# Kernel tuning notes

Measured on AMD Instinct MI355X. Metric: run time of the kernel, lower is better.

Reference implementation:

```python
import jax, jax.numpy as jnp
import numpy as np

B, T, N, NIN = 2, 10, 128, 6
K, H = 4, 128          # edge_types, n_hid
E = N * (N - 1)        # fully-connected, no self-loops


def _linear_init(key, out_f, in_f, bias=True):
    k1, k2 = jax.random.split(key)
    bound = 1.0 / np.sqrt(in_f)
    W = jax.random.uniform(k1, (out_f, in_f), jnp.float32, -bound, bound)
    if bias:
        b = jax.random.uniform(k2, (out_f,), jnp.float32, -bound, bound)
        return W, b
    return W


def setup_inputs() -> dict:
    key = jax.random.key(0)
    ks = jax.random.split(key, 20)
    # graph structure: one-hot receiver/sender matrices (NRI style)
    off_diag = np.ones((N, N), dtype=np.float32) - np.eye(N, dtype=np.float32)
    send_idx, recv_idx = np.where(off_diag)
    eye = np.eye(N, dtype=np.float32)
    rel_rec = jnp.asarray(eye[recv_idx])   # [E, N]
    rel_send = jnp.asarray(eye[send_idx])  # [E, N]

    data = jax.random.normal(ks[0], (B, T, N, NIN), jnp.float32)
    rel_type = jax.nn.softmax(jax.random.normal(ks[1], (B, E, K), jnp.float32), axis=-1)

    # per-edge-type message MLPs, stacked over edge type
    m1 = [_linear_init(ks[2 + i], H, 2 * H) for i in range(K)]
    m2 = [_linear_init(ks[6 + i], H, H) for i in range(K)]
    W_msg1 = jnp.stack([w for w, _ in m1]); b_msg1 = jnp.stack([b for _, b in m1])
    W_msg2 = jnp.stack([w for w, _ in m2]); b_msg2 = jnp.stack([b for _, b in m2])

    W_hr = _linear_init(ks[10], H, H, bias=False)
    W_hi = _linear_init(ks[11], H, H, bias=False)
    W_hh = _linear_init(ks[12], H, H, bias=False)
    W_ir, b_ir = _linear_init(ks[13], H, NIN)
    W_ii, b_ii = _linear_init(ks[14], H, NIN)
    W_in, b_in = _linear_init(ks[15], H, NIN)
    W_o1, b_o1 = _linear_init(ks[16], H, H)
    W_o2, b_o2 = _linear_init(ks[17], H, H)
    W_o3, b_o3 = _linear_init(ks[18], NIN, H)

    return dict(data=data, rel_type=rel_type, rel_rec=rel_rec, rel_send=rel_send,
                W_msg1=W_msg1, b_msg1=b_msg1, W_msg2=W_msg2, b_msg2=b_msg2,
                W_hr=W_hr, W_hi=W_hi, W_hh=W_hh,
                W_ir=W_ir, b_ir=b_ir, W_ii=W_ii, b_ii=b_ii, W_in=W_in, b_in=b_in,
                W_o1=W_o1, b_o1=b_o1, W_o2=W_o2, b_o2=b_o2, W_o3=W_o3, b_o3=b_o3)


def reference(data, rel_type, rel_rec, rel_send,
              W_msg1, b_msg1, W_msg2, b_msg2,
              W_hr, W_hi, W_hh,
              W_ir, b_ir, W_ii, b_ii, W_in, b_in,
              W_o1, b_o1, W_o2, b_o2, W_o3, b_o3):
    norm = float(K)  # skip_first=False -> all edge types, norm = edge_types
    rel_type_k = jnp.transpose(rel_type, (2, 0, 1))[..., None]  # [K, B, E, 1]

    def single_step(hidden, ins):
        # gather node hidden states to edges
        receivers = jnp.einsum('en,bnh->beh', rel_rec, hidden)
        senders = jnp.einsum('en,bnh->beh', rel_send, hidden)
        pre_msg = jnp.concatenate([receivers, senders], axis=-1)  # [B, E, 2H]
        # per-edge-type 2-layer tanh MLP, batched over edge types (dropout p=0)
        msg = jnp.tanh(jnp.einsum('bef,khf->kbeh', pre_msg, W_msg1) + b_msg1[:, None, None, :])
        msg = jnp.tanh(jnp.einsum('kbeh,kgh->kbeg', msg, W_msg2) + b_msg2[:, None, None, :])
        all_msgs = jnp.sum(msg * rel_type_k, axis=0) / norm      # [B, E, H]
        # scatter-aggregate edge messages to receiver nodes
        agg = jnp.einsum('beh,en->bnh', all_msgs, rel_rec) / NIN  # [B, N, H]
        # GRU-style update
        r = jax.nn.sigmoid(ins @ W_ir.T + b_ir + agg @ W_hr.T)
        i = jax.nn.sigmoid(ins @ W_ii.T + b_ii + agg @ W_hi.T)
        n = jnp.tanh(ins @ W_in.T + b_in + r * (agg @ W_hh.T))
        hidden_new = (1.0 - i) * n + i * hidden
        # output MLP with residual (dropout p=0)
        p = jax.nn.relu(hidden_new @ W_o1.T + b_o1)
        p = jax.nn.relu(p @ W_o2.T + b_o2)
        pred = ins + p @ W_o3.T + b_o3
        return hidden_new, pred

    hidden0 = jnp.zeros((B, N, H), data.dtype)
    # pred_steps=1 (default) -> every step consumes the ground-truth frame
    ins_seq = jnp.transpose(data[:, :-1], (1, 0, 2, 3))  # [T-1, B, N, NIN]
    _, preds = jax.lax.scan(single_step, hidden0, ins_seq)
    # stack(dim=1).transpose(1,2) -> [B, N, T-1, NIN]
    return jnp.transpose(preds, (1, 2, 0, 3))
```

## Files before the change

### kernel.cpp

```cpp
#include <hip/hip_runtime.h>

#define NN 128
#define HH 128
#define BB 2
#define KT 4
#define EE 16256
#define TT 9

typedef __bf16 v8bf __attribute__((ext_vector_type(8)));
typedef float v4f __attribute__((ext_vector_type(4)));

__device__ __forceinline__ float tanh_fast(float x) {
  return 1.0f - __fdividef(2.0f, __expf(2.0f * x) + 1.0f);
}
__device__ __forceinline__ float sigmoid_fast(float x) {
  return __fdividef(1.0f, 1.0f + __expf(-x));
}
__device__ __forceinline__ unsigned short f2bf(float f) {
  unsigned int u = __float_as_uint(f);
  u += 0x7FFFu + ((u >> 16) & 1u);
  return (unsigned short)(u >> 16);
}

__global__ void prep_kernel(const float* __restrict__ W_msg1,
                            const float* __restrict__ W_msg2,
                            float* __restrict__ W1T,
                            unsigned short* __restrict__ W2bf) {
  int idx = blockIdx.x * 256 + threadIdx.x;
  int ku = idx >> 14, h = (idx >> 7) & 127, g = idx & 127;
  int k = ku >> 1, u = ku & 1;
  W1T[idx] = W_msg1[(k * 128 + g) * 256 + u * 128 + h];
  if (idx < 65536) W2bf[idx] = f2bf(W_msg2[idx]);
}

__global__ __launch_bounds__(512)
void step_kernel(const float* __restrict__ data,
                 const float* __restrict__ rel_type,
                 const float* __restrict__ b_msg1,
                 const float* __restrict__ b_msg2,
                 const float* __restrict__ W_hr,
                 const float* __restrict__ W_hi,
                 const float* __restrict__ W_hh,
                 const float* __restrict__ W_ir, const float* __restrict__ b_ir,
                 const float* __restrict__ W_ii, const float* __restrict__ b_ii,
                 const float* __restrict__ W_in, const float* __restrict__ b_in,
                 const float* __restrict__ W_o1, const float* __restrict__ b_o1,
                 const float* __restrict__ W_o2, const float* __restrict__ b_o2,
                 const float* __restrict__ W_o3, const float* __restrict__ b_o3,
                 const float* __restrict__ W1T,
                 const unsigned short* __restrict__ W2bf,
                 float* __restrict__ hidden,
                 const float* __restrict__ UVin,
                 float* __restrict__ UVout,
                 float* __restrict__ outp,
                 int t) {
  __shared__ unsigned short msg1_lds[16384];
  __shared__ unsigned short w2_lds[16384];
  __shared__ float ub_lds[128];
  __shared__ float rel_lds[128];
  __shared__ float b2_lds[128];
  __shared__ float colsum[8][128];
  __shared__ float agg_lds[128];
  __shared__ float hid_lds[128];
  __shared__ float hn_lds[128];
  __shared__ float ins_lds[6];
  __shared__ float g_r[128], g_i[128], g_hh[128], g_in[128];
  __shared__ float p1_lds[128], p2_lds[128];

  const int tid = threadIdx.x;
  const int lane = tid & 63;
  const int wave = tid >> 6;
  const int b = blockIdx.x >> 7;
  const int n = blockIdx.x & 127;

  float acc_all[8][4];
#pragma unroll
  for (int c = 0; c < 8; ++c)
#pragma unroll
    for (int r = 0; r < 4; ++r) acc_all[c][r] = 0.f;

  for (int k = 0; k < KT; ++k) {
    const uint4* w2g4 = (const uint4*)(W2bf + k * 16384);
#pragma unroll
    for (int c = 0; c < 4; ++c) {
      int chunk = tid + c * 512;
      int row = chunk >> 4, cc = chunk & 15;
      uint4 v = w2g4[chunk];
      int off = (row << 8) + (cc << 4);
      off ^= (row & 7) << 4;
      *(uint4*)((char*)w2_lds + off) = v;
    }
    if (tid < 128) {
      ub_lds[tid] = UVin[(((k * 2 + 0) * BB + b) * NN + n) * HH + tid] + b_msg1[k * 128 + tid];
      b2_lds[tid] = b_msg2[k * 128 + tid];
      float rv = 0.f;
      int r = tid;
      if (r != n) {
        int e = r * 127 + (n < r ? n : n - 1);
        rv = rel_type[(b * EE + e) * KT + k];
      }
      rel_lds[r] = rv;
    }
    __syncthreads();

    {
      int r = tid >> 2;
      int h0 = (tid & 3) << 5;
      const float4* vrow = (const float4*)(UVin + (((k * 2 + 1) * BB + b) * NN + r) * HH + h0);
#pragma unroll
      for (int m = 0; m < 4; ++m) {
        float4 va = vrow[m * 2];
        float4 vb = vrow[m * 2 + 1];
        int hb = h0 + m * 8;
        unsigned int p0 = (unsigned)f2bf(tanh_fast(ub_lds[hb + 0] + va.x)) |
                          ((unsigned)f2bf(tanh_fast(ub_lds[hb + 1] + va.y)) << 16);
        unsigned int p1 = (unsigned)f2bf(tanh_fast(ub_lds[hb + 2] + va.z)) |
                          ((unsigned)f2bf(tanh_fast(ub_lds[hb + 3] + va.w)) << 16);
        unsigned int p2 = (unsigned)f2bf(tanh_fast(ub_lds[hb + 4] + vb.x)) |
                          ((unsigned)f2bf(tanh_fast(ub_lds[hb + 5] + vb.y)) << 16);
        unsigned int p3 = (unsigned)f2bf(tanh_fast(ub_lds[hb + 6] + vb.z)) |
                          ((unsigned)f2bf(tanh_fast(ub_lds[hb + 7] + vb.w)) << 16);
        uint4 pk;
        pk.x = p0; pk.y = p1; pk.z = p2; pk.w = p3;
        int off = (r << 8) + (hb << 1);
        off ^= (r & 7) << 4;
        *(uint4*)((char*)msg1_lds + off) = pk;
      }
    }
    __syncthreads();

    v4f acck[8];
#pragma unroll
    for (int c = 0; c < 8; ++c) acck[c] = (v4f){0.f, 0.f, 0.f, 0.f};
#pragma unroll
    for (int ks = 0; ks < 4; ++ks) {
      int ar = wave * 16 + (lane & 15);
      int ac = ks * 64 + ((lane >> 4) << 4);
      int aoff = (ar << 8) + ac;
      aoff ^= (ar & 7) << 4;
      v8bf afrag = *(const v8bf*)((const char*)msg1_lds + aoff);
#pragma unroll
      for (int c = 0; c < 8; ++c) {
        int br = c * 16 + (lane & 15);
        int boff = (br << 8) + ac;
        boff ^= (br & 7) << 4;
        v8bf bfrag = *(const v8bf*)((const char*)w2_lds + boff);
        acck[c] = __builtin_amdgcn_mfma_f32_16x16x32_bf16(afrag, bfrag, acck[c], 0, 0, 0);
      }
    }
#pragma unroll
    for (int c = 0; c < 8; ++c) {
      float bb = b2_lds[c * 16 + (lane & 15)];
#pragma unroll
      for (int rg = 0; rg < 4; ++rg) {
        int rowg = wave * 16 + ((lane >> 4) << 2) + rg;
        float v = tanh_fast(acck[c][rg] + bb);
        acc_all[c][rg] += v * rel_lds[rowg];
      }
    }
    __syncthreads();
  }

#pragma unroll
  for (int c = 0; c < 8; ++c) {
    float s = acc_all[c][0] + acc_all[c][1] + acc_all[c][2] + acc_all[c][3];
    s += __shfl_xor(s, 16);
    s += __shfl_xor(s, 32);
    if ((lane >> 4) == 0) colsum[wave][c * 16 + lane] = s;
  }
  __syncthreads();
  if (tid < 128) {
    float s = 0.f;
#pragma unroll
    for (int w = 0; w < 8; ++w) s += colsum[w][tid];
    agg_lds[tid] = s * (1.0f / 24.0f);
    hid_lds[tid] = hidden[(b * NN + n) * HH + tid];
  }
  if (tid >= 128 && tid < 134) ins_lds[tid - 128] = data[((b * 10 + t) * NN + n) * 6 + (tid - 128)];
  __syncthreads();

  {
    int h = tid >> 2, q = tid & 3;
    const float4* whr = (const float4*)(W_hr + h * 128 + q * 32);
    const float4* whi = (const float4*)(W_hi + h * 128 + q * 32);
    const float4* whh = (const float4*)(W_hh + h * 128 + q * 32);
    const float4* ag4 = (const float4*)(agg_lds + q * 32);
    float phr = 0.f, phi = 0.f, phh = 0.f;
#pragma unroll
    for (int j = 0; j < 8; ++j) {
      float4 a = ag4[j];
      float4 wr = whr[j], wi = whi[j], wh = whh[j];
      phr += wr.x * a.x + wr.y * a.y + wr.z * a.z + wr.w * a.w;
      phi += wi.x * a.x + wi.y * a.y + wi.z * a.z + wi.w * a.w;
      phh += wh.x * a.x + wh.y * a.y + wh.z * a.z + wh.w * a.w;
    }
    phr += __shfl_xor(phr, 1); phr += __shfl_xor(phr, 2);
    phi += __shfl_xor(phi, 1); phi += __shfl_xor(phi, 2);
    phh += __shfl_xor(phh, 1); phh += __shfl_xor(phh, 2);
    if (q == 0) {
      float dr = b_ir[h], di = b_ii[h], dn = b_in[h];
#pragma unroll
      for (int j = 0; j < 6; ++j) {
        float iv = ins_lds[j];
        dr += W_ir[h * 6 + j] * iv;
        di += W_ii[h * 6 + j] * iv;
        dn += W_in[h * 6 + j] * iv;
      }
      g_r[h] = dr + phr; g_i[h] = di + phi; g_hh[h] = phh; g_in[h] = dn;
    }
  }
  __syncthreads();
  if (tid < 128) {
    float r = sigmoid_fast(g_r[tid]);
    float ii = sigmoid_fast(g_i[tid]);
    float ng = tanh_fast(g_in[tid] + r * g_hh[tid]);
    float hn = (1.0f - ii) * ng + ii * hid_lds[tid];
    hn_lds[tid] = hn;
    hidden[(b * NN + n) * HH + tid] = hn;
  }
  __syncthreads();

  {
    int h = tid >> 2, q = tid & 3;
    const float4* w4 = (const float4*)(W_o1 + h * 128 + q * 32);
    const float4* a4 = (const float4*)(hn_lds + q * 32);
    float p = 0.f;
#pragma unroll
    for (int j = 0; j < 8; ++j) {
      float4 w = w4[j]; float4 a = a4[j];
      p += w.x * a.x + w.y * a.y + w.z * a.z + w.w * a.w;
    }
    p += __shfl_xor(p, 1); p += __shfl_xor(p, 2);
    if (q == 0) p1_lds[h] = fmaxf(p + b_o1[h], 0.f);
  }
  __syncthreads();
  {
    int h = tid >> 2, q = tid & 3;
    const float4* w4 = (const float4*)(W_o2 + h * 128 + q * 32);
    const float4* a4 = (const float4*)(p1_lds + q * 32);
    float p = 0.f;
#pragma unroll
    for (int j = 0; j < 8; ++j) {
      float4 w = w4[j]; float4 a = a4[j];
      p += w.x * a.x + w.y * a.y + w.z * a.z + w.w * a.w;
    }
    p += __shfl_xor(p, 1); p += __shfl_xor(p, 2);
    if (q == 0) p2_lds[h] = fmaxf(p + b_o2[h], 0.f);
  }
  __syncthreads();
  if (tid < 48) {
    int i = tid >> 3, oc = tid & 7;
    const float4* w4 = (const float4*)(W_o3 + i * 128 + oc * 16);
    const float4* a4 = (const float4*)(p2_lds + oc * 16);
    float p = 0.f;
#pragma unroll
    for (int j = 0; j < 4; ++j) {
      float4 w = w4[j]; float4 a = a4[j];
      p += w.x * a.x + w.y * a.y + w.z * a.z + w.w * a.w;
    }
    p += __shfl_xor(p, 1); p += __shfl_xor(p, 2); p += __shfl_xor(p, 4);
    if (oc == 0) outp[((b * NN + n) * TT + t) * 6 + i] = ins_lds[i] + p + b_o3[i];
  }

#pragma unroll
  for (int it = 0; it < 2; ++it) {
    int idx = tid + it * 512;
    int kh = idx >> 7, g = idx & 127;
    const float* wcol = W1T + kh * 16384 + g;
    float s = 0.f;
#pragma unroll 8
    for (int h = 0; h < 128; ++h) s += wcol[h * 128] * hn_lds[h];
    UVout[((kh * BB + b) * NN + n) * HH + g] = s;
  }
}

extern "C" void kernel_launch(void* const* d_in, const int* in_sizes, int n_in,
                              void* d_out, int out_size, void* d_ws, size_t ws_size,
                              hipStream_t stream) {
  const float* data     = (const float*)d_in[0];
  const float* rel_type = (const float*)d_in[1];
  const float* W_msg1 = (const float*)d_in[4];
  const float* b_msg1 = (const float*)d_in[5];
  const float* W_msg2 = (const float*)d_in[6];
  const float* b_msg2 = (const float*)d_in[7];
  const float* W_hr = (const float*)d_in[8];
  const float* W_hi = (const float*)d_in[9];
  const float* W_hh = (const float*)d_in[10];
  const float* W_ir = (const float*)d_in[11];
  const float* b_ir = (const float*)d_in[12];
  const float* W_ii = (const float*)d_in[13];
  const float* b_ii = (const float*)d_in[14];
  const float* W_in = (const float*)d_in[15];
  const float* b_in = (const float*)d_in[16];
  const float* W_o1 = (const float*)d_in[17];
  const float* b_o1 = (const float*)d_in[18];
  const float* W_o2 = (const float*)d_in[19];
  const float* b_o2 = (const float*)d_in[20];
  const float* W_o3 = (const float*)d_in[21];
  const float* b_o3 = (const float*)d_in[22];
  float* outp = (float*)d_out;

  char* ws = (char*)d_ws;
  float* hidden = (float*)(ws);
  float* UVa    = (float*)(ws + 131072);
  float* UVb    = (float*)(ws + 131072 + 1048576);
  float* W1T    = (float*)(ws + 131072 + 2097152);
  unsigned short* W2bf = (unsigned short*)(ws + 131072 + 2097152 + 524288);

  hipMemsetAsync(hidden, 0, 131072, stream);
  hipMemsetAsync(UVa, 0, 1048576, stream);
  prep_kernel<<<512, 256, 0, stream>>>(W_msg1, W_msg2, W1T, W2bf);

  for (int t = 0; t < TT; ++t) {
    float* uvin = (t & 1) ? UVb : UVa;
    float* uvout = (t & 1) ? UVa : UVb;
    step_kernel<<<BB * NN, 512, 0, stream>>>(
        data, rel_type, b_msg1, b_msg2, W_hr, W_hi, W_hh,
        W_ir, b_ir, W_ii, b_ii, W_in, b_in,
        W_o1, b_o1, W_o2, b_o2, W_o3, b_o3,
        W1T, W2bf, hidden, uvin, uvout, outp, t);
  }
}
```

Before: 514.8 us.

## Stage all W2 in LDS once, build A fragments in registers, MFMA for UV projection

Loads all four edge-type W2 matrices into LDS once per block (128 KB), removing the per-edge-type reload and the two barriers inside the k-loop. The first-layer message activations are computed straight into MFMA A fragments in registers instead of going through LDS. The rel_type gather is precomputed into a dense per-node table in the prep kernel. The per-step U/V projection of the new hidden state moves from a scalar fp32 loop to bf16 MFMA with hi/lo split compensation to keep accuracy. Risks: 128 KB+ of LDS lowers occupancy to one block per CU, and the MFMA GEMV wastes 15/16 of the A rows.

```diff
diff --git a/kernel.cpp b/kernel.cpp
--- a/kernel.cpp
+++ b/kernel.cpp
@@ -24,22 +24,39 @@
 
 __global__ void prep_kernel(const float* __restrict__ W_msg1,
                             const float* __restrict__ W_msg2,
-                            float* __restrict__ W1T,
-                            unsigned short* __restrict__ W2bf) {
+                            const float* __restrict__ rel_type,
+                            unsigned short* __restrict__ W1hi,
+                            unsigned short* __restrict__ W1lo,
+                            unsigned short* __restrict__ W2bf,
+                            float* __restrict__ relp) {
   int idx = blockIdx.x * 256 + threadIdx.x;
-  int ku = idx >> 14, h = (idx >> 7) & 127, g = idx & 127;
-  int k = ku >> 1, u = ku & 1;
-  W1T[idx] = W_msg1[(k * 128 + g) * 256 + u * 128 + h];
+  {
+    int h = idx & 127, g = (idx >> 7) & 127, ku = idx >> 14;
+    int k = ku >> 1, u = ku & 1;
+    float w = W_msg1[(k * 128 + g) * 256 + u * 128 + h];
+    unsigned short hi = f2bf(w);
+    float whi = __uint_as_float(((unsigned int)hi) << 16);
+    W1hi[idx] = hi;
+    W1lo[idx] = f2bf(w - whi);
+  }
   if (idx < 65536) W2bf[idx] = f2bf(W_msg2[idx]);
+  {
+    int r = idx & 127, k = (idx >> 7) & 3, n = (idx >> 9) & 127, b = idx >> 16;
+    float v = 0.f;
+    if (r != n) {
+      int e = r * 127 + (n < r ? n : n - 1);
+      v = rel_type[(b * EE + e) * KT + k];
+    }
+    relp[idx] = v;
+  }
 }
 
 __global__ __launch_bounds__(512)
 void step_kernel(const float* __restrict__ data,
-                 const float* __restrict__ rel_type,
                  const float* __restrict__ b_msg1,
                  const float* __restrict__ b_msg2,
                  const float* __restrict__ W_hr,
-                 const float* __restrict__ W_hi,
+                 const float* __restrict__ W_hi_,
                  const float* __restrict__ W_hh,
                  const float* __restrict__ W_ir, const float* __restrict__ b_ir,
                  const float* __restrict__ W_ii, const float* __restrict__ b_ii,
@@ -47,18 +64,19 @@
                  const float* __restrict__ W_o1, const float* __restrict__ b_o1,
                  const float* __restrict__ W_o2, const float* __restrict__ b_o2,
                  const float* __restrict__ W_o3, const float* __restrict__ b_o3,
-                 const float* __restrict__ W1T,
+                 const unsigned short* __restrict__ W1hi,
+                 const unsigned short* __restrict__ W1lo,
                  const unsigned short* __restrict__ W2bf,
+                 const float* __restrict__ relp,
                  float* __restrict__ hidden,
                  const float* __restrict__ UVin,
                  float* __restrict__ UVout,
                  float* __restrict__ outp,
                  int t) {
-  __shared__ unsigned short msg1_lds[16384];
-  __shared__ unsigned short w2_lds[16384];
-  __shared__ float ub_lds[128];
-  __shared__ float rel_lds[128];
-  __shared__ float b2_lds[128];
+  __shared__ unsigned short w2_lds[65536];
+  __shared__ float ub_lds[512];
+  __shared__ float b2_lds[512];
+  __shared__ float rel_lds[512];
   __shared__ float colsum[8][128];
   __shared__ float agg_lds[128];
   __shared__ float hid_lds[128];
@@ -73,6 +91,25 @@
   const int b = blockIdx.x >> 7;
   const int n = blockIdx.x & 127;
 
+  {
+    const uint4* w2g = (const uint4*)W2bf;
+#pragma unroll
+    for (int i = 0; i < 16; ++i) {
+      int cid = tid + i * 512;
+      int plane = cid >> 11, c2 = cid & 2047;
+      int g = c2 >> 4, cc = c2 & 15;
+      uint4 v = w2g[cid];
+      int off = (plane << 15) + (g << 8) + (cc << 4);
+      off ^= (g & 7) << 4;
+      *(uint4*)((char*)w2_lds + off) = v;
+    }
+    int k = tid >> 7, h = tid & 127;
+    ub_lds[tid] = UVin[(((k * 2 + 0) * BB + b) * NN + n) * HH + h] + b_msg1[tid];
+    b2_lds[tid] = b_msg2[tid];
+    rel_lds[tid] = relp[(b * NN + n) * (KT * NN) + tid];
+  }
+  __syncthreads();
+
   float acc_all[8][4];
 #pragma unroll
   for (int c = 0; c < 8; ++c)
@@ -80,85 +117,48 @@
     for (int r = 0; r < 4; ++r) acc_all[c][r] = 0.f;
 
   for (int k = 0; k < KT; ++k) {
-    const uint4* w2g4 = (const uint4*)(W2bf + k * 16384);
-#pragma unroll
-    for (int c = 0; c < 4; ++c) {
-      int chunk = tid + c * 512;
-      int row = chunk >> 4, cc = chunk & 15;
-      uint4 v = w2g4[chunk];
-      int off = (row << 8) + (cc << 4);
-      off ^= (row & 7) << 4;
-      *(uint4*)((char*)w2_lds + off) = v;
-    }
-    if (tid < 128) {
-      ub_lds[tid] = UVin[(((k * 2 + 0) * BB + b) * NN + n) * HH + tid] + b_msg1[k * 128 + tid];
-      b2_lds[tid] = b_msg2[k * 128 + tid];
-      float rv = 0.f;
-      int r = tid;
-      if (r != n) {
-        int e = r * 127 + (n < r ? n : n - 1);
-        rv = rel_type[(b * EE + e) * KT + k];
-      }
-      rel_lds[r] = rv;
-    }
-    __syncthreads();
-
-    {
-      int r = tid >> 2;
-      int h0 = (tid & 3) << 5;
-      const float4* vrow = (const float4*)(UVin + (((k * 2 + 1) * BB + b) * NN + r) * HH + h0);
-#pragma unroll
-      for (int m = 0; m < 4; ++m) {
-        float4 va = vrow[m * 2];
-        float4 vb = vrow[m * 2 + 1];
-        int hb = h0 + m * 8;
-        unsigned int p0 = (unsigned)f2bf(tanh_fast(ub_lds[hb + 0] + va.x)) |
-                          ((unsigned)f2bf(tanh_fast(ub_lds[hb + 1] + va.y)) << 16);
-        unsigned int p1 = (unsigned)f2bf(tanh_fast(ub_lds[hb + 2] + va.z)) |
-                          ((unsigned)f2bf(tanh_fast(ub_lds[hb + 3] + va.w)) << 16);
-        unsigned int p2 = (unsigned)f2bf(tanh_fast(ub_lds[hb + 4] + vb.x)) |
-                          ((unsigned)f2bf(tanh_fast(ub_lds[hb + 5] + vb.y)) << 16);
-        unsigned int p3 = (unsigned)f2bf(tanh_fast(ub_lds[hb + 6] + vb.z)) |
-                          ((unsigned)f2bf(tanh_fast(ub_lds[hb + 7] + vb.w)) << 16);
-        uint4 pk;
-        pk.x = p0; pk.y = p1; pk.z = p2; pk.w = p3;
-        int off = (r << 8) + (hb << 1);
-        off ^= (r & 7) << 4;
-        *(uint4*)((char*)msg1_lds + off) = pk;
-      }
-    }
-    __syncthreads();
-
+    const float* vbase = UVin + (((k * 2 + 1) * BB + b) * NN + (wave * 16 + (lane & 15))) * HH;
+    v8bf af[4];
+#pragma unroll
+    for (int ks = 0; ks < 4; ++ks) {
+      int c0 = ks * 32 + ((lane >> 4) << 3);
+      float4 v0 = *(const float4*)(vbase + c0);
+      float4 v1 = *(const float4*)(vbase + c0 + 4);
+      const float* up = ub_lds + k * 128 + c0;
+      float4 u0 = *(const float4*)(up);
+      float4 u1 = *(const float4*)(up + 4);
+      af[ks][0] = (__bf16)tanh_fast(u0.x + v0.x);
+      af[ks][1] = (__bf16)tanh_fast(u0.y + v0.y);
+      af[ks][2] = (__bf16)tanh_fast(u0.z + v0.z);
+      af[ks][3] = (__bf16)tanh_fast(u0.w + v0.w);
+      af[ks][4] = (__bf16)tanh_fast(u1.x + v1.x);
+      af[ks][5] = (__bf16)tanh_fast(u1.y + v1.y);
+      af[ks][6] = (__bf16)tanh_fast(u1.z + v1.z);
+      af[ks][7] = (__bf16)tanh_fast(u1.w + v1.w);
+    }
     v4f acck[8];
 #pragma unroll
     for (int c = 0; c < 8; ++c) acck[c] = (v4f){0.f, 0.f, 0.f, 0.f};
 #pragma unroll
     for (int ks = 0; ks < 4; ++ks) {
-      int ar = wave * 16 + (lane & 15);
-      int ac = ks * 64 + ((lane >> 4) << 4);
-      int aoff = (ar << 8) + ac;
-      aoff ^= (ar & 7) << 4;
-      v8bf afrag = *(const v8bf*)((const char*)msg1_lds + aoff);
 #pragma unroll
       for (int c = 0; c < 8; ++c) {
-        int br = c * 16 + (lane & 15);
-        int boff = (br << 8) + ac;
-        boff ^= (br & 7) << 4;
+        int g = c * 16 + (lane & 15);
+        int boff = (k << 15) + (g << 8) + (ks << 6) + ((lane >> 4) << 4);
+        boff ^= (g & 7) << 4;
         v8bf bfrag = *(const v8bf*)((const char*)w2_lds + boff);
-        acck[c] = __builtin_amdgcn_mfma_f32_16x16x32_bf16(afrag, bfrag, acck[c], 0, 0, 0);
+        acck[c] = __builtin_amdgcn_mfma_f32_16x16x32_bf16(af[ks], bfrag, acck[c], 0, 0, 0);
       }
     }
 #pragma unroll
     for (int c = 0; c < 8; ++c) {
-      float bb = b2_lds[c * 16 + (lane & 15)];
+      float bb = b2_lds[k * 128 + c * 16 + (lane & 15)];
 #pragma unroll
       for (int rg = 0; rg < 4; ++rg) {
         int rowg = wave * 16 + ((lane >> 4) << 2) + rg;
-        float v = tanh_fast(acck[c][rg] + bb);
-        acc_all[c][rg] += v * rel_lds[rowg];
-      }
-    }
-    __syncthreads();
+        acc_all[c][rg] += tanh_fast(acck[c][rg] + bb) * rel_lds[k * 128 + rowg];
+      }
+    }
   }
 
 #pragma unroll
@@ -182,7 +182,7 @@
   {
     int h = tid >> 2, q = tid & 3;
     const float4* whr = (const float4*)(W_hr + h * 128 + q * 32);
-    const float4* whi = (const float4*)(W_hi + h * 128 + q * 32);
+    const float4* whi = (const float4*)(W_hi_ + h * 128 + q * 32);
     const float4* whh = (const float4*)(W_hh + h * 128 + q * 32);
     const float4* ag4 = (const float4*)(agg_lds + q * 32);
     float phr = 0.f, phi = 0.f, phh = 0.f;
@@ -262,15 +262,38 @@
     if (oc == 0) outp[((b * NN + n) * TT + t) * 6 + i] = ins_lds[i] + p + b_o3[i];
   }
 
-#pragma unroll
-  for (int it = 0; it < 2; ++it) {
-    int idx = tid + it * 512;
-    int kh = idx >> 7, g = idx & 127;
-    const float* wcol = W1T + kh * 16384 + g;
-    float s = 0.f;
-#pragma unroll 8
-    for (int h = 0; h < 128; ++h) s += wcol[h * 128] * hn_lds[h];
-    UVout[((kh * BB + b) * NN + n) * HH + g] = s;
+  {
+    v8bf hf_hi[4], hf_lo[4];
+#pragma unroll
+    for (int q = 0; q < 4; ++q) {
+      int c0 = q * 32 + ((lane >> 4) << 3);
+      bool live = (lane & 15) == 0;
+#pragma unroll
+      for (int j = 0; j < 8; ++j) {
+        float a = live ? hn_lds[c0 + j] : 0.f;
+        __bf16 ah = (__bf16)a;
+        hf_hi[q][j] = ah;
+        hf_lo[q][j] = (__bf16)(a - (float)ah);
+      }
+    }
+#pragma unroll
+    for (int c = 0; c < 8; ++c) {
+      int gg = (wave * 8 + c) * 16 + (lane & 15);
+      v4f acc = (v4f){0.f, 0.f, 0.f, 0.f};
+#pragma unroll
+      for (int q = 0; q < 4; ++q) {
+        int hoff = q * 32 + ((lane >> 4) << 3);
+        v8bf bhi = *(const v8bf*)(W1hi + (size_t)gg * 128 + hoff);
+        v8bf blo = *(const v8bf*)(W1lo + (size_t)gg * 128 + hoff);
+        acc = __builtin_amdgcn_mfma_f32_16x16x32_bf16(hf_hi[q], bhi, acc, 0, 0, 0);
+        acc = __builtin_amdgcn_mfma_f32_16x16x32_bf16(hf_lo[q], bhi, acc, 0, 0, 0);
+        acc = __builtin_amdgcn_mfma_f32_16x16x32_bf16(hf_hi[q], blo, acc, 0, 0, 0);
+      }
+      if ((lane >> 4) == 0) {
+        int kh = gg >> 7, g = gg & 127;
+        UVout[((kh * BB + b) * NN + n) * HH + g] = acc[0];
+      }
+    }
   }
 }
 
@@ -301,23 +324,25 @@
   float* outp = (float*)d_out;
 
   char* ws = (char*)d_ws;
-  float* hidden = (float*)(ws);
-  float* UVa    = (float*)(ws + 131072);
-  float* UVb    = (float*)(ws + 131072 + 1048576);
-  float* W1T    = (float*)(ws + 131072 + 2097152);
-  unsigned short* W2bf = (unsigned short*)(ws + 131072 + 2097152 + 524288);
+  float* hidden        = (float*)(ws);
+  float* UVa           = (float*)(ws + 131072);
+  float* UVb           = (float*)(ws + 1179648);
+  unsigned short* W1hi = (unsigned short*)(ws + 2228224);
+  unsigned short* W1lo = (unsigned short*)(ws + 2490368);
+  unsigned short* W2bf = (unsigned short*)(ws + 2752512);
+  float* relp          = (float*)(ws + 2883584);
 
   hipMemsetAsync(hidden, 0, 131072, stream);
   hipMemsetAsync(UVa, 0, 1048576, stream);
-  prep_kernel<<<512, 256, 0, stream>>>(W_msg1, W_msg2, W1T, W2bf);
+  prep_kernel<<<512, 256, 0, stream>>>(W_msg1, W_msg2, rel_type, W1hi, W1lo, W2bf, relp);
 
   for (int t = 0; t < TT; ++t) {
     float* uvin = (t & 1) ? UVb : UVa;
     float* uvout = (t & 1) ? UVa : UVb;
     step_kernel<<<BB * NN, 512, 0, stream>>>(
-        data, rel_type, b_msg1, b_msg2, W_hr, W_hi, W_hh,
+        data, b_msg1, b_msg2, W_hr, W_hi, W_hh,
         W_ir, b_ir, W_ii, b_ii, W_in, b_in,
         W_o1, b_o1, W_o2, b_o2, W_o3, b_o3,
-        W1T, W2bf, hidden, uvin, uvout, outp, t);
-  }
-}
+        W1hi, W1lo, W2bf, relp, hidden, uvin, uvout, outp, t);
+  }
+}
```

New measurement: 583.0 us. 1.13x slower.
